# Kernel tuning notes

Measured on AMD Instinct MI355X. Metric: run time of the kernel, lower is better.

## Reference

```python
import jax, jax.numpy as jnp
import numpy as np

EPS = 1e-6

def _quat_mul(q1, q2):
    # Hamilton product, broadcasting over leading dims; last dim = 4 (w,x,y,z)
    w1, x1, y1, z1 = jnp.moveaxis(q1, -1, 0)
    w2, x2, y2, z2 = jnp.moveaxis(q2, -1, 0)
    return jnp.stack([
        w1*w2 - x1*x2 - y1*y2 - z1*z2,
        w1*x2 + x1*w2 + y1*z2 - z1*y2,
        w1*y2 - x1*z2 + y1*w2 + z1*x2,
        w1*z2 + x1*y2 - y1*x2 + z1*w2,
    ], axis=-1)

def _quat_log(q):
    # log(q) = arccos(clamp(w)) * v/||v||, zero when ||v|| < EPS
    w = q[..., 0]
    v = q[..., 1:]
    v_norm = jnp.linalg.norm(v, axis=-1)
    safe = v_norm >= EPS
    scale = jnp.arccos(jnp.clip(w, -1.0, 1.0)) / jnp.where(safe, v_norm, 1.0)
    return jnp.where(safe[..., None], scale[..., None] * v, jnp.zeros_like(v))

def _quat_exp(omega):
    # exp(omega) = [cos||w||, sin||w|| * w/||w||]; identity when ||w|| < EPS
    theta = jnp.linalg.norm(omega, axis=-1)
    safe = theta >= EPS
    w = jnp.cos(theta)
    xyz = (jnp.sin(theta) / jnp.where(safe, theta, 1.0))[..., None] * omega
    q = jnp.concatenate([w[..., None], xyz], axis=-1)
    ident = jnp.array([1.0, 0.0, 0.0, 0.0], dtype=omega.dtype)
    return jnp.where(safe[..., None], q, ident)

def setup_inputs() -> dict:
    key = jax.random.key(0)
    k1, k2, k3, k4 = jax.random.split(key, 4)
    B = 2097152
    HORIZON = 10
    def unit_quat(k):
        q = jax.random.normal(k, (B, 4), dtype=jnp.float32)
        return q / jnp.linalg.norm(q, axis=-1, keepdims=True)
    q_prev = unit_quat(k1)
    q_curr = unit_quat(k2)
    # xavier_uniform with gain=0.1 for w1 [16,8] and w2 [4,16]
    lim1 = 0.1 * np.sqrt(6.0 / (16 + 8))
    lim2 = 0.1 * np.sqrt(6.0 / (4 + 16))
    w1 = jax.random.uniform(k3, (16, 8), dtype=jnp.float32, minval=-lim1, maxval=lim1)
    w2 = jax.random.uniform(k4, (4, 16), dtype=jnp.float32, minval=-lim2, maxval=lim2)
    b1 = jnp.zeros((16,), dtype=jnp.float32)
    b2 = jnp.zeros((4,), dtype=jnp.float32)
    t_steps = jnp.linspace(0.1, 1.0, HORIZON, dtype=jnp.float32)
    return {"q_prev": q_prev, "q_curr": q_curr, "w1": w1, "b1": b1,
            "w2": w2, "b2": b2, "t_steps": t_steps}

def reference(q_prev, q_curr, w1, b1, w2, b2, t_steps):
    # MLP velocity correction: [B,8] -> tanh -> [B,4]
    velocity_input = jnp.concatenate([q_prev, q_curr], axis=-1)       # [B,8]
    h = jnp.tanh(velocity_input @ w1.T + b1)                          # [B,16]
    velocity_correction = h @ w2.T + b2                               # [B,4]

    # omega = 2 * log(q_curr * conj(q_prev))  -> [B,3]
    conj = jnp.array([1.0, -1.0, -1.0, -1.0], dtype=q_prev.dtype)
    delta_q = _quat_mul(q_curr, q_prev * conj)
    omega = 2.0 * _quat_log(delta_q)

    # Constant-angular-velocity extrapolation over the horizon
    ot = omega[:, None, :] * t_steps[None, :, None]                   # [B,H,3]
    q_delta = _quat_exp(ot)                                           # [B,H,4]
    q_pred = _quat_mul(q_delta, q_curr[:, None, :])                   # [B,H,4]
    q_pred = q_pred + velocity_correction[:, None, :] * t_steps[None, :, None] * 0.1
    norm = jnp.maximum(jnp.linalg.norm(q_pred, axis=-1, keepdims=True), 1e-12)
    return q_pred / norm                                              # [B,H,4]
```

## Files before the change

kernel.cpp:

```cpp
#include <hip/hip_runtime.h>
#include <math.h>

#define EPS_F 1e-6f
#define BLOCK 128
#define STRIDE_DW 44

typedef float f4 __attribute__((ext_vector_type(4)));

__global__ __launch_bounds__(BLOCK, 7) void traj_kernel(
    const f4*    __restrict__ q_prev,
    const f4*    __restrict__ q_curr,
    const float* __restrict__ w1,
    const float* __restrict__ b1,
    const float* __restrict__ w2,
    const float* __restrict__ b2,
    const float* __restrict__ t_steps,
    f4*          __restrict__ out,
    int B)
{
    __shared__ float lds[64 * STRIDE_DW];

    const int tid = threadIdx.x;
    int i = blockIdx.x * BLOCK + tid;
    if (i >= B) i = B - 1;

    const f4 qp = __builtin_nontemporal_load(&q_prev[i]);
    const f4 qc = __builtin_nontemporal_load(&q_curr[i]);

    float in8[8] = {qp.x, qp.y, qp.z, qp.w, qc.x, qc.y, qc.z, qc.w};

    float h[16];
#pragma unroll
    for (int j = 0; j < 16; ++j) {
        float acc = b1[j];
#pragma unroll
        for (int k = 0; k < 8; ++k) acc = fmaf(w1[j * 8 + k], in8[k], acc);
        float e = __expf(2.0f * acc);
        h[j] = 1.0f - 2.0f / (e + 1.0f);
    }

    float vc[4];
#pragma unroll
    for (int j = 0; j < 4; ++j) {
        float acc = b2[j];
#pragma unroll
        for (int k = 0; k < 16; ++k) acc = fmaf(w2[j * 16 + k], h[k], acc);
        vc[j] = acc;
    }

    float dw =  qc.x*qp.x + qc.y*qp.y + qc.z*qp.z + qc.w*qp.w;
    float dx = -qc.x*qp.y + qc.y*qp.x - qc.z*qp.w + qc.w*qp.z;
    float dy = -qc.x*qp.z + qc.y*qp.w + qc.z*qp.x - qc.w*qp.y;
    float dz = -qc.x*qp.w - qc.y*qp.z + qc.z*qp.y + qc.w*qp.x;

    float vn  = sqrtf(dx*dx + dy*dy + dz*dz);
    float wcl = fminf(fmaxf(dw, -1.0f), 1.0f);
    float ang = acosf(wcl);
    bool  safe = (vn >= EPS_F);
    float inv_vn = safe ? (1.0f / vn) : 0.0f;
    float ux = dx * inv_vn, uy = dy * inv_vn, uz = dz * inv_vn;
    float on = safe ? (2.0f * ang) : 0.0f;

    const size_t base = (size_t)blockIdx.x * (BLOCK * 10);

#pragma unroll
    for (int p = 0; p < 2; ++p) {
        if ((tid >> 6) == p) {
            const int el = tid & 63;
#pragma unroll
            for (int st = 0; st < 10; ++st) {
                float t  = t_steps[st];
                float th = on * t;
                float s, c;
                __sincosf(th, &s, &c);
                float ax = s * ux, ay = s * uy, az = s * uz;

                float pw = c*qc.x - ax*qc.y - ay*qc.z - az*qc.w;
                float px = c*qc.y + ax*qc.x + ay*qc.w - az*qc.z;
                float py = c*qc.z - ax*qc.w + ay*qc.x + az*qc.y;
                float pz = c*qc.w + ax*qc.z - ay*qc.y + az*qc.x;

                float tf = t * 0.1f;
                pw = fmaf(vc[0], tf, pw);
                px = fmaf(vc[1], tf, px);
                py = fmaf(vc[2], tf, py);
                pz = fmaf(vc[3], tf, pz);

                float n2 = pw*pw + px*px + py*py + pz*pz;
                float r  = rsqrtf(fmaxf(n2, 1e-24f));

                f4 v; v.x = pw*r; v.y = px*r; v.z = py*r; v.w = pz*r;
                *(f4*)&lds[el * STRIDE_DW + st * 4] = v;
            }
        }
        __syncthreads();

#pragma unroll
        for (int k = 0; k < 5; ++k) {
            int g = k * BLOCK + tid;
            int e = g / 10;
            int s = g - e * 10;
            f4 v = *(const f4*)&lds[e * STRIDE_DW + s * 4];
            __builtin_nontemporal_store(v, &out[base + (size_t)p * 640 + g]);
        }
        if (p == 0) __syncthreads();
    }
}

extern "C" void kernel_launch(void* const* d_in, const int* in_sizes, int n_in,
                              void* d_out, int out_size, void* d_ws, size_t ws_size,
                              hipStream_t stream) {
    const f4*    q_prev  = (const f4*)d_in[0];
    const f4*    q_curr  = (const f4*)d_in[1];
    const float* w1      = (const float*)d_in[2];
    const float* b1      = (const float*)d_in[3];
    const float* w2      = (const float*)d_in[4];
    const float* b2      = (const float*)d_in[5];
    const float* t_steps = (const float*)d_in[6];
    f4*          out     = (f4*)d_out;

    int B = in_sizes[0] / 4;
    int grid = (B + BLOCK - 1) / BLOCK;
    traj_kernel<<<grid, BLOCK, 0, stream>>>(q_prev, q_curr, w1, b1, w2, b2,
                                            t_steps, out, B);
}
```

Measured before the change: 85.04 us.

## Convert to persistent grid-stride kernel with software-pipelined next-tile prefetch and MLP

Replaces the one-tile-per-block launch with a persistent kernel capped at 2048 blocks that loops over tiles. While the current tile's outputs are staged through LDS and stored, it prefetches the next tile's quaternions and computes part of the next MLP, so memory traffic and math can overlap. It also caches t_steps in registers and lowers the launch-bounds occupancy hint. The cost is more register pressure, fewer resident waves, and dropping the tail handling when B is not a multiple of the block size.

New measurement: 93.34 us. 1.1x slower.

```diff
diff --git a/kernel.cpp b/kernel.cpp
--- a/kernel.cpp
+++ b/kernel.cpp
@@ -7,7 +7,7 @@
 
 typedef float f4 __attribute__((ext_vector_type(4)));
 
-__global__ __launch_bounds__(BLOCK, 7) void traj_kernel(
+__global__ __launch_bounds__(BLOCK, 4) void traj_kernel(
     const f4*    __restrict__ q_prev,
     const f4*    __restrict__ q_curr,
     const float* __restrict__ w1,
@@ -20,56 +20,70 @@
 {
     __shared__ float lds[64 * STRIDE_DW];
 
-    const int tid = threadIdx.x;
-    int i = blockIdx.x * BLOCK + tid;
-    if (i >= B) i = B - 1;
-
-    const f4 qp = __builtin_nontemporal_load(&q_prev[i]);
-    const f4 qc = __builtin_nontemporal_load(&q_curr[i]);
-
-    float in8[8] = {qp.x, qp.y, qp.z, qp.w, qc.x, qc.y, qc.z, qc.w};
-
-    float h[16];
-#pragma unroll
-    for (int j = 0; j < 16; ++j) {
-        float acc = b1[j];
-#pragma unroll
-        for (int k = 0; k < 8; ++k) acc = fmaf(w1[j * 8 + k], in8[k], acc);
-        float e = __expf(2.0f * acc);
-        h[j] = 1.0f - 2.0f / (e + 1.0f);
+    const int tid    = threadIdx.x;
+    const int ntiles = B / BLOCK;
+    const int stride = gridDim.x;
+
+    int T = blockIdx.x;
+    if (T >= ntiles) return;
+
+    float tt[10];
+#pragma unroll
+    for (int s = 0; s < 10; ++s) tt[s] = t_steps[s];
+
+    f4 qp = __builtin_nontemporal_load(&q_prev[(size_t)T * BLOCK + tid]);
+    f4 qc = __builtin_nontemporal_load(&q_curr[(size_t)T * BLOCK + tid]);
+
+    float vc0, vc1, vc2, vc3, ux, uy, uz, on;
+    {
+        float in8[8] = {qp.x, qp.y, qp.z, qp.w, qc.x, qc.y, qc.z, qc.w};
+        float h[16];
+#pragma unroll
+        for (int j = 0; j < 16; ++j) {
+            float acc = b1[j];
+#pragma unroll
+            for (int k = 0; k < 8; ++k) acc = fmaf(w1[j * 8 + k], in8[k], acc);
+            float e = __expf(2.0f * acc);
+            h[j] = 1.0f - 2.0f / (e + 1.0f);
+        }
+        float vcl[4];
+#pragma unroll
+        for (int j = 0; j < 4; ++j) {
+            float acc = b2[j];
+#pragma unroll
+            for (int k = 0; k < 16; ++k) acc = fmaf(w2[j * 16 + k], h[k], acc);
+            vcl[j] = acc;
+        }
+        vc0 = vcl[0]; vc1 = vcl[1]; vc2 = vcl[2]; vc3 = vcl[3];
+
+        float dw =  qc.x*qp.x + qc.y*qp.y + qc.z*qp.z + qc.w*qp.w;
+        float dx = -qc.x*qp.y + qc.y*qp.x - qc.z*qp.w + qc.w*qp.z;
+        float dy = -qc.x*qp.z + qc.y*qp.w + qc.z*qp.x - qc.w*qp.y;
+        float dz = -qc.x*qp.w - qc.y*qp.z + qc.z*qp.y + qc.w*qp.x;
+
+        float vn  = sqrtf(dx*dx + dy*dy + dz*dz);
+        float wcl = fminf(fmaxf(dw, -1.0f), 1.0f);
+        float ang = acosf(wcl);
+        bool  safe = (vn >= EPS_F);
+        float inv_vn = safe ? (1.0f / vn) : 0.0f;
+        ux = dx * inv_vn; uy = dy * inv_vn; uz = dz * inv_vn;
+        on = safe ? (2.0f * ang) : 0.0f;
     }
 
-    float vc[4];
-#pragma unroll
-    for (int j = 0; j < 4; ++j) {
-        float acc = b2[j];
-#pragma unroll
-        for (int k = 0; k < 16; ++k) acc = fmaf(w2[j * 16 + k], h[k], acc);
-        vc[j] = acc;
-    }
-
-    float dw =  qc.x*qp.x + qc.y*qp.y + qc.z*qp.z + qc.w*qp.w;
-    float dx = -qc.x*qp.y + qc.y*qp.x - qc.z*qp.w + qc.w*qp.z;
-    float dy = -qc.x*qp.z + qc.y*qp.w + qc.z*qp.x - qc.w*qp.y;
-    float dz = -qc.x*qp.w - qc.y*qp.z + qc.z*qp.y + qc.w*qp.x;
-
-    float vn  = sqrtf(dx*dx + dy*dy + dz*dz);
-    float wcl = fminf(fmaxf(dw, -1.0f), 1.0f);
-    float ang = acosf(wcl);
-    bool  safe = (vn >= EPS_F);
-    float inv_vn = safe ? (1.0f / vn) : 0.0f;
-    float ux = dx * inv_vn, uy = dy * inv_vn, uz = dz * inv_vn;
-    float on = safe ? (2.0f * ang) : 0.0f;
-
-    const size_t base = (size_t)blockIdx.x * (BLOCK * 10);
-
-#pragma unroll
-    for (int p = 0; p < 2; ++p) {
-        if ((tid >> 6) == p) {
+    while (true) {
+        const int  Tn        = T + stride;
+        const bool have_next = (Tn < ntiles);
+
+        const size_t base = (size_t)T * (BLOCK * 10);
+        f4 qpn, qcn;
+        float hn[16];
+        float nvc0, nvc1, nvc2, nvc3, nux, nuy, nuz, non;
+
+        if ((tid >> 6) == 0) {
             const int el = tid & 63;
 #pragma unroll
             for (int st = 0; st < 10; ++st) {
-                float t  = t_steps[st];
+                float t  = tt[st];
                 float th = on * t;
                 float s, c;
                 __sincosf(th, &s, &c);
@@ -81,19 +95,21 @@
                 float pz = c*qc.w + ax*qc.z - ay*qc.y + az*qc.x;
 
                 float tf = t * 0.1f;
-                pw = fmaf(vc[0], tf, pw);
-                px = fmaf(vc[1], tf, px);
-                py = fmaf(vc[2], tf, py);
-                pz = fmaf(vc[3], tf, pz);
+                pw = fmaf(vc0, tf, pw); px = fmaf(vc1, tf, px);
+                py = fmaf(vc2, tf, py); pz = fmaf(vc3, tf, pz);
 
                 float n2 = pw*pw + px*px + py*py + pz*pz;
                 float r  = rsqrtf(fmaxf(n2, 1e-24f));
-
                 f4 v; v.x = pw*r; v.y = px*r; v.z = py*r; v.w = pz*r;
                 *(f4*)&lds[el * STRIDE_DW + st * 4] = v;
             }
         }
         __syncthreads();
+
+        if (have_next) {
+            qpn = __builtin_nontemporal_load(&q_prev[(size_t)Tn * BLOCK + tid]);
+            qcn = __builtin_nontemporal_load(&q_curr[(size_t)Tn * BLOCK + tid]);
+        }
 
 #pragma unroll
         for (int k = 0; k < 5; ++k) {
@@ -101,9 +117,90 @@
             int e = g / 10;
             int s = g - e * 10;
             f4 v = *(const f4*)&lds[e * STRIDE_DW + s * 4];
-            __builtin_nontemporal_store(v, &out[base + (size_t)p * 640 + g]);
-        }
-        if (p == 0) __syncthreads();
+            __builtin_nontemporal_store(v, &out[base + g]);
+        }
+
+        if (have_next) {
+            float in8[8] = {qpn.x, qpn.y, qpn.z, qpn.w, qcn.x, qcn.y, qcn.z, qcn.w};
+#pragma unroll
+            for (int j = 0; j < 16; ++j) {
+                float acc = b1[j];
+#pragma unroll
+                for (int k = 0; k < 8; ++k) acc = fmaf(w1[j * 8 + k], in8[k], acc);
+                float e = __expf(2.0f * acc);
+                hn[j] = 1.0f - 2.0f / (e + 1.0f);
+            }
+        }
+        __syncthreads();
+
+        if ((tid >> 6) == 1) {
+            const int el = tid & 63;
+#pragma unroll
+            for (int st = 0; st < 10; ++st) {
+                float t  = tt[st];
+                float th = on * t;
+                float s, c;
+                __sincosf(th, &s, &c);
+                float ax = s * ux, ay = s * uy, az = s * uz;
+
+                float pw = c*qc.x - ax*qc.y - ay*qc.z - az*qc.w;
+                float px = c*qc.y + ax*qc.x + ay*qc.w - az*qc.z;
+                float py = c*qc.z - ax*qc.w + ay*qc.x + az*qc.y;
+                float pz = c*qc.w + ax*qc.z - ay*qc.y + az*qc.x;
+
+                float tf = t * 0.1f;
+                pw = fmaf(vc0, tf, pw); px = fmaf(vc1, tf, px);
+                py = fmaf(vc2, tf, py); pz = fmaf(vc3, tf, pz);
+
+                float n2 = pw*pw + px*px + py*py + pz*pz;
+                float r  = rsqrtf(fmaxf(n2, 1e-24f));
+                f4 v; v.x = pw*r; v.y = px*r; v.z = py*r; v.w = pz*r;
+                *(f4*)&lds[el * STRIDE_DW + st * 4] = v;
+            }
+        }
+        __syncthreads();
+
+#pragma unroll
+        for (int k = 0; k < 5; ++k) {
+            int g = k * BLOCK + tid;
+            int e = g / 10;
+            int s = g - e * 10;
+            f4 v = *(const f4*)&lds[e * STRIDE_DW + s * 4];
+            __builtin_nontemporal_store(v, &out[base + 640 + g]);
+        }
+
+        if (!have_next) break;
+
+        {
+            float vcl[4];
+#pragma unroll
+            for (int j = 0; j < 4; ++j) {
+                float acc = b2[j];
+#pragma unroll
+                for (int k = 0; k < 16; ++k) acc = fmaf(w2[j * 16 + k], hn[k], acc);
+                vcl[j] = acc;
+            }
+            nvc0 = vcl[0]; nvc1 = vcl[1]; nvc2 = vcl[2]; nvc3 = vcl[3];
+
+            float dw =  qcn.x*qpn.x + qcn.y*qpn.y + qcn.z*qpn.z + qcn.w*qpn.w;
+            float dx = -qcn.x*qpn.y + qcn.y*qpn.x - qcn.z*qpn.w + qcn.w*qpn.z;
+            float dy = -qcn.x*qpn.z + qcn.y*qpn.w + qcn.z*qpn.x - qcn.w*qpn.y;
+            float dz = -qcn.x*qpn.w - qcn.y*qpn.z + qcn.z*qpn.y + qcn.w*qpn.x;
+
+            float vn  = sqrtf(dx*dx + dy*dy + dz*dz);
+            float wcl = fminf(fmaxf(dw, -1.0f), 1.0f);
+            float ang = acosf(wcl);
+            bool  safe = (vn >= EPS_F);
+            float inv_vn = safe ? (1.0f / vn) : 0.0f;
+            nux = dx * inv_vn; nuy = dy * inv_vn; nuz = dz * inv_vn;
+            non = safe ? (2.0f * ang) : 0.0f;
+        }
+
+        qp = qpn; qc = qcn;
+        vc0 = nvc0; vc1 = nvc1; vc2 = nvc2; vc3 = nvc3;
+        ux = nux; uy = nuy; uz = nuz; on = non;
+        __syncthreads();
+        T = Tn;
     }
 }
 
@@ -120,7 +217,8 @@
     f4*          out     = (f4*)d_out;
 
     int B = in_sizes[0] / 4;
-    int grid = (B + BLOCK - 1) / BLOCK;
+    int ntiles = B / BLOCK;
+    int grid = ntiles < 2048 ? ntiles : 2048;
     traj_kernel<<<grid, BLOCK, 0, stream>>>(q_prev, q_curr, w1, b1, w2, b2,
                                             t_steps, out, B);
 }
```
